# Performance work log

Measured on AMD Instinct MI355X. Metric: run time of the kernel, lower is better.

Reference implementation:

```python
import jax, jax.numpy as jnp
import numpy as np

H = 16   # num_heads
G = 4    # groups (code structurally requires 4)
DIM = 1024
HD = DIM // H // G  # 16


def setup_inputs() -> dict:
    key = jax.random.key(0)
    k1, k2, k3 = jax.random.split(key, 3)
    x = jax.random.normal(k1, (8, 4096, DIM), dtype=jnp.float32)
    w_qkvw = jax.random.normal(k2, (DIM, 4 * DIM), dtype=jnp.float32) * 0.02
    w_out = jax.random.normal(k3, (DIM, DIM), dtype=jnp.float32) * 0.02
    return {"x": x, "w_qkvw": w_qkvw, "w_out": w_out}


def reference(x, w_qkvw, w_out):
    B, S, dim = x.shape
    qkvw = x @ w_qkvw  # [B, S, 4*dim]
    # chunk into G groups along last dim -> G tensors of [B, S, dim] (G==4)
    chunks = jnp.split(qkvw, G, axis=-1)
    # each chunk split again into G sub-chunks of [B, S, dim/G]
    subs = [jnp.split(t, G, axis=-1) for t in chunks]
    # torch: q,k,v,w = [cat([qi,ki,vi,wi], dim=0) for qi,ki,vi,wi in zip(*subs)]
    q = jnp.concatenate([subs[i][0] for i in range(4)], axis=0)  # [4B, S, dim/G]
    k = jnp.concatenate([subs[i][1] for i in range(4)], axis=0)
    v = jnp.concatenate([subs[i][2] for i in range(4)], axis=0)
    w = jnp.concatenate([subs[i][3] for i in range(4)], axis=0)
    # faithful row-major reshape: [4B, S, dim/G] -> [4B, H, S, hd] -> transpose(1,2)
    def shp(t):
        return t.reshape(B * G, H, -1, HD).swapaxes(1, 2)  # [4B, S, H, hd]
    q, k, v = shp(q), shp(k), shp(v)
    w = w.reshape(B * G, H, -1, HD)  # [4B, H, S, hd]
    scale = HD ** -0.5
    scores = (q @ k.swapaxes(-2, -1)) * scale          # [4B, S, H, H]
    attn = jax.nn.softmax(scores, axis=-1)
    o = (attn @ v).swapaxes(1, 2).reshape(B, S, dim)   # [B, S, dim]
    return (o * w.reshape(B, S, dim)) @ w_out
```

## Files before the change

kernel.cpp:

```cpp
#include <hip/hip_runtime.h>
#include <hip/hip_bf16.h>
#include <stdint.h>


typedef __bf16 bf16;
typedef __bf16 bf16x8 __attribute__((ext_vector_type(8)));
typedef float f32x4 __attribute__((ext_vector_type(4)));

__device__ __forceinline__ void gload16(const bf16* g, bf16* l) {
  __builtin_amdgcn_global_load_lds(
      (const __attribute__((address_space(1))) void*)g,
      (__attribute__((address_space(3))) void*)l, 16, 0, 0);
}

#define BAR() __builtin_amdgcn_s_barrier()
#define SB() __builtin_amdgcn_sched_barrier(0)
#define LGKM0 asm volatile("s_waitcnt lgkmcnt(0)" ::: "memory")
#define VM6 asm volatile("s_waitcnt vmcnt(6)" ::: "memory")
#define VM0 asm volatile("s_waitcnt vmcnt(0)" ::: "memory")
#define PRIO1 __builtin_amdgcn_s_setprio(1)
#define PRIO0 __builtin_amdgcn_s_setprio(0)

#define READ_A8(dst, base, mq)                                                \
  {                                                                           \
    _Pragma("unroll") for (int i = 0; i < 4; ++i)                             \
        _Pragma("unroll") for (int kk = 0; kk < 2; ++kk)                      \
            dst[i][kk] = *(const bf16x8*)(lds + (base) + ahalf +              \
                                          ((mq)*64 + i * 16 + fr) * 128 +     \
                                          ((kk * 64 + fkb) ^ xo));            \
  }
#define READ_B4(dst, base, nh)                                                \
  {                                                                           \
    _Pragma("unroll") for (int j2 = 0; j2 < 2; ++j2)                          \
        _Pragma("unroll") for (int kk = 0; kk < 2; ++kk)                      \
            dst[j2][kk] = *(const bf16x8*)(lds + (base) + bhalf +             \
                                           (bro + (nh)*32 + j2 * 16 + fr) * 128 + \
                                           ((kk * 64 + fkb) ^ xo));           \
  }
#define MFMA_Q(arr, bv, mq, nh)                                               \
  {                                                                           \
    _Pragma("unroll") for (int i = 0; i < 4; ++i)                             \
        _Pragma("unroll") for (int j2 = 0; j2 < 2; ++j2) {                    \
      acc[(mq)*4 + i][(nh)*2 + j2] = __builtin_amdgcn_mfma_f32_16x16x32_bf16( \
          arr[i][0], bv[j2][0], acc[(mq)*4 + i][(nh)*2 + j2], 0, 0, 0);       \
      acc[(mq)*4 + i][(nh)*2 + j2] = __builtin_amdgcn_mfma_f32_16x16x32_bf16( \
          arr[i][1], bv[j2][1], acc[(mq)*4 + i][(nh)*2 + j2], 0, 0, 0);       \
    }                                                                         \
  }
#define STAGE(gsrc, lbase)                                                    \
  {                                                                           \
    gload16((gsrc), (bf16*)(lds + (lbase) + wv * 1024));                      \
    gload16((gsrc) + 64 * 1024, (bf16*)(lds + (lbase) + 8192 + wv * 1024));   \
  }

template <typename OutT>
__global__ __launch_bounds__(512, 2)
void gemm256(const bf16* __restrict__ A, const bf16* __restrict__ BT,
             OutT* __restrict__ C, int N, int super) {
  constexpr int K = 1024;
  __shared__ __align__(16) char smem[131072];
  char* lds = smem;

  const int tid = threadIdx.x;
  const int lane = tid & 63;
  const int wv = tid >> 6;
  const int wr = wv >> 2;
  const int wc = wv & 3;

  const int gx = gridDim.x;
  const int nwg = gx * gridDim.y;
  const int bid = blockIdx.y * gx + blockIdx.x;
  const int xcd = bid & 7;
  const int l = bid >> 3;
  long trow, tcol;
  if (super) {
    const int s = l >> 5, i = l & 31;
    const int colS = gx >> 2;
    trow = xcd * 16 + (s / colS) * 8 + (i >> 2);
    tcol = (s % colS) * 4 + (i & 3);
  } else {
    const int swz = xcd * (nwg >> 3) + l;
    trow = swz / gx;
    tcol = swz % gx;
  }
  const long row0 = trow * 256;
  const long col0 = tcol * 256;

  const int srow = tid >> 3;
  const int scol = (((tid & 7) * 16) ^ ((srow & 7) << 4)) >> 1;
  const bf16* gA = A + (row0 + srow) * K + scol;
  const bf16* gB = BT + (col0 + srow) * K + scol;

  const int fr = lane & 15;
  const int fkb = (lane >> 4) * 16;
  const int xo = (fr & 7) << 4;
  const int bro = (wc & 1) * 64;
  const int ahalf = wr * 16384;
  const int bhalf = (wc >> 1) * 16384;

  bf16x8 a0[4][2], a1[4][2], bn0[2][2], bn1[2][2];
  f32x4 acc[8][4] = {};

  STAGE(gA, 0); STAGE(gA + 131072, 16384);
  STAGE(gB, 65536); STAGE(gB + 131072, 81920);
  STAGE(gB + 64, 98304); STAGE(gB + 131072 + 64, 114688);
  STAGE(gA + 64, 32768);
  VM6;
  BAR();

  const bf16* gAm = gA;
  const bf16* gBm = gB;
  for (int j = 0; j < 8; ++j) {
    const bool nl = (j < 7);
    READ_B4(bn0, 65536, 0);
    STAGE(gAm + 131072 + 64, 49152);
    BAR(); LGKM0; SB();
    if (j) { PRIO1; MFMA_Q(a1, bn1, 1, 1); PRIO0; }
    BAR();
    READ_A8(a0, 0, 0);
    READ_B4(bn1, 65536, 1);
    BAR(); LGKM0; SB();
    PRIO1; MFMA_Q(a0, bn0, 0, 0); PRIO0;
    BAR();
    READ_A8(a1, 0, 1);
    if (nl) { STAGE(gBm + 128, 65536); STAGE(gBm + 131072 + 128, 81920); }
    BAR(); LGKM0; SB();
    PRIO1; MFMA_Q(a1, bn0, 1, 0); PRIO0;
    BAR();
    if (nl) {
      STAGE(gAm + 128, 0);
      VM6;
    } else {
      VM0;
    }
    BAR(); LGKM0; SB();
    PRIO1; MFMA_Q(a0, bn1, 0, 1); PRIO0;
    BAR();
    READ_B4(bn0, 98304, 0);
    if (nl) STAGE(gAm + 131072 + 128, 16384);
    BAR(); LGKM0; SB();
    PRIO1; MFMA_Q(a1, bn1, 1, 1); PRIO0;
    BAR();
    READ_A8(a0, 32768, 0);
    READ_B4(bn1, 98304, 1);
    BAR(); LGKM0; SB();
    PRIO1; MFMA_Q(a0, bn0, 0, 0); PRIO0;
    BAR();
    READ_A8(a1, 32768, 1);
    if (nl) STAGE(gBm + 192, 98304);
    BAR(); LGKM0; SB();
    PRIO1; MFMA_Q(a1, bn0, 1, 0); PRIO0;
    BAR();
    if (nl) {
      STAGE(gBm + 131072 + 192, 114688);
      STAGE(gAm + 192, 32768);
      VM6;
    }
    BAR(); LGKM0; SB();
    PRIO1; MFMA_Q(a0, bn1, 0, 1); PRIO0;
    BAR();
    gAm += 128;
    gBm += 128;
  }
  PRIO1; MFMA_Q(a1, bn1, 1, 1); PRIO0;

  const int crow = (lane >> 4) * 4;
  const int ccol = lane & 15;
  const long rb = row0 + wr * 128;
  const long cb = col0 + wc * 64;
#pragma unroll
  for (int m = 0; m < 8; ++m)
#pragma unroll
    for (int n = 0; n < 4; ++n)
#pragma unroll
      for (int i = 0; i < 4; ++i)
        C[(rb + m * 16 + crow + i) * (long)N + cb + n * 16 + ccol] =
            (OutT)acc[m][n][i];
}

__device__ __forceinline__ void load16f(const bf16* p, float* f) {
  const uint4* u = (const uint4*)p;
  uint4 a = u[0], b = u[1];
  uint32_t w[8] = {a.x, a.y, a.z, a.w, b.x, b.y, b.z, b.w};
#pragma unroll
  for (int j = 0; j < 8; ++j) {
    f[2 * j] = __uint_as_float(w[j] << 16);
    f[2 * j + 1] = __uint_as_float(w[j] & 0xffff0000u);
  }
}

__global__ __launch_bounds__(256)
void attn_fuse(const bf16* __restrict__ qkvw, bf16* __restrict__ ow,
               int b0, long bstride) {
  __shared__ bf16 data[16 * 1024];
  const int s_hi = blockIdx.x;
  const int g = blockIdx.y;
  const int bz = blockIdx.z;
  const int b = b0 + bz;
  const bf16* base = qkvw + (long)bz * bstride;
  const int tid = threadIdx.x;

#pragma unroll
  for (int i = 0; i < 8; ++i) {
    int c = tid + i * 256;
    int h = c >> 7;
    int col = (c & 127) * 8;
    *(uint4*)&data[h * 1024 + col] =
        *(const uint4*)(base + (long)(h * 256 + s_hi) * 4096 + g * 1024 + col);
  }
  __syncthreads();

  const int s_lo = tid >> 4;
  const int h1 = tid & 15;
  const int off = s_lo * 16;

  float q[16], p[16], o[16];
  load16f(&data[h1 * 1024 + off], q);

  float mx = -1e30f;
#pragma unroll
  for (int h2 = 0; h2 < 16; ++h2) {
    float kf[16];
    load16f(&data[h2 * 1024 + 256 + off], kf);
    float s = 0.f;
#pragma unroll
    for (int d = 0; d < 16; ++d) s += q[d] * kf[d];
    s *= 0.25f;
    p[h2] = s;
    mx = fmaxf(mx, s);
  }
  float sum = 0.f;
#pragma unroll
  for (int h2 = 0; h2 < 16; ++h2) {
    float e = __expf(p[h2] - mx);
    p[h2] = e;
    sum += e;
  }
  const float inv = 1.f / sum;
#pragma unroll
  for (int d = 0; d < 16; ++d) o[d] = 0.f;
#pragma unroll
  for (int h2 = 0; h2 < 16; ++h2) {
    float vf[16];
    load16f(&data[h2 * 1024 + 512 + off], vf);
    const float av = p[h2] * inv;
#pragma unroll
    for (int d = 0; d < 16; ++d) o[d] += av * vf[d];
  }
  float wf[16];
  load16f(&data[h1 * 1024 + 768 + off], wf);

  const int bp = g * 8 + b;
  const long R = (long)(bp >> 2) * 4096 + (bp & 3) * 1024 + h1 * 64 + (s_hi >> 2);
  const int cbo = (s_hi & 3) * 256 + off;
  union { uint4 u[2]; bf16 hh[16]; } st;
#pragma unroll
  for (int d = 0; d < 16; ++d) st.hh[d] = (bf16)(o[d] * wf[d]);
  uint4* dst = (uint4*)&ow[R * 1024 + cbo];
  dst[0] = st.u[0];
  dst[1] = st.u[1];
}

__global__ __launch_bounds__(256)
void cast_x_kernel(const float* __restrict__ in, bf16* __restrict__ out, long n4) {
  long i = (long)blockIdx.x * 256 + threadIdx.x;
  if (i >= n4) return;
  float4 v = ((const float4*)in)[i];
  union { uint2 d; bf16 h[4]; } r;
  r.h[0] = (bf16)v.x; r.h[1] = (bf16)v.y; r.h[2] = (bf16)v.z; r.h[3] = (bf16)v.w;
  ((uint2*)out)[i] = r.d;
}

__global__ __launch_bounds__(256)
void tcast_kernel(const float* __restrict__ in, bf16* __restrict__ out, int R, int C) {
  __shared__ float t[64][65];
  const int c0 = blockIdx.x * 64, r0 = blockIdx.y * 64;
  const int lr = threadIdx.x >> 6;
  const int lc = threadIdx.x & 63;
#pragma unroll
  for (int i = 0; i < 16; ++i)
    t[lr + i * 4][lc] = in[(long)(r0 + lr + i * 4) * C + c0 + lc];
  __syncthreads();
#pragma unroll
  for (int i = 0; i < 16; ++i) {
    int oc = lr + i * 4;
    out[(long)(c0 + oc) * R + r0 + lc] = (bf16)t[lc][oc];
  }
}

extern "C" void kernel_launch(void* const* d_in, const int* in_sizes, int n_in,
                              void* d_out, int out_size, void* d_ws, size_t ws_size,
                              hipStream_t stream) {
  const float* x = (const float*)d_in[0];
  const float* w_qkvw = (const float*)d_in[1];
  const float* w_out = (const float*)d_in[2];
  float* out = (float*)d_out;

  char* ws = (char*)d_ws;
  size_t off = 0;
  bf16* x_bf = (bf16*)(ws + off); off += (size_t)32768 * 1024 * 2;
  bf16* bt1  = (bf16*)(ws + off); off += (size_t)4096 * 1024 * 2;
  bf16* bt2  = (bf16*)(ws + off); off += (size_t)1024 * 1024 * 2;
  bf16* owb  = (bf16*)(ws + off); off += (size_t)32768 * 1024 * 2;
  bf16* qk   = (bf16*)(ws + off);
  const size_t rem = ws_size > off ? ws_size - off : 0;
  const size_t full_need = (size_t)32768 * 4096 * 2;

  cast_x_kernel<<<32768, 256, 0, stream>>>(x, x_bf, (long)8388608);
  tcast_kernel<<<dim3(64, 16), 256, 0, stream>>>(w_qkvw, bt1, 1024, 4096);
  tcast_kernel<<<dim3(16, 16), 256, 0, stream>>>(w_out, bt2, 1024, 1024);

  if (rem >= full_need) {
    gemm256<bf16><<<dim3(16, 128), 512, 0, stream>>>(x_bf, bt1, qk, 4096, 1);
    attn_fuse<<<dim3(256, 4, 8), 256, 0, stream>>>(qk, owb, 0, (long)4096 * 4096);
  } else {
    for (int b = 0; b < 8; ++b) {
      gemm256<bf16><<<dim3(16, 16), 512, 0, stream>>>(
          x_bf + (size_t)b * 4096 * 1024, bt1, qk, 4096, 0);
      attn_fuse<<<dim3(256, 4, 1), 256, 0, stream>>>(qk, owb, b, 0);
    }
  }
  gemm256<float><<<dim3(4, 128), 512, 0, stream>>>(owb, bt2, out, 1024, 1);
}
```

Measured before the change: 506.2 us.

## Restructure GEMM main loop with fewer barriers and partial LDS waitcnts

Reorders the K-loop so all A fragments for a half-tile are read up front, uses partial lgkmcnt waits (8/4/0) so MFMAs start before every LDS read completes, and removes about half the workgroup barriers. The global-to-LDS staging order is reshuffled, with B's second half now prefetched inside the loop and vmcnt lowered to 4. This cuts synchronization stalls and improves overlap of LDS reads with MFMA, but the tighter buffer reuse risks LDS read/write hazards and higher register pressure.

```diff
diff --git a/kernel.cpp b/kernel.cpp
--- a/kernel.cpp
+++ b/kernel.cpp
@@ -15,8 +15,10 @@
 
 #define BAR() __builtin_amdgcn_s_barrier()
 #define SB() __builtin_amdgcn_sched_barrier(0)
+#define LGKM8 asm volatile("s_waitcnt lgkmcnt(8)" ::: "memory")
+#define LGKM4 asm volatile("s_waitcnt lgkmcnt(4)" ::: "memory")
 #define LGKM0 asm volatile("s_waitcnt lgkmcnt(0)" ::: "memory")
-#define VM6 asm volatile("s_waitcnt vmcnt(6)" ::: "memory")
+#define VM4 asm volatile("s_waitcnt vmcnt(4)" ::: "memory")
 #define VM0 asm volatile("s_waitcnt vmcnt(0)" ::: "memory")
 #define PRIO1 __builtin_amdgcn_s_setprio(1)
 #define PRIO0 __builtin_amdgcn_s_setprio(0)
@@ -103,66 +105,64 @@
 
   STAGE(gA, 0); STAGE(gA + 131072, 16384);
   STAGE(gB, 65536); STAGE(gB + 131072, 81920);
-  STAGE(gB + 64, 98304); STAGE(gB + 131072 + 64, 114688);
-  STAGE(gA + 64, 32768);
-  VM6;
-  BAR();
+  STAGE(gA + 64, 32768); STAGE(gA + 131072 + 64, 49152);
+  VM4;
 
   const bf16* gAm = gA;
   const bf16* gBm = gB;
   for (int j = 0; j < 8; ++j) {
     const bool nl = (j < 7);
+    BAR();
     READ_B4(bn0, 65536, 0);
-    STAGE(gAm + 131072 + 64, 49152);
-    BAR(); LGKM0; SB();
-    if (j) { PRIO1; MFMA_Q(a1, bn1, 1, 1); PRIO0; }
-    BAR();
     READ_A8(a0, 0, 0);
+    READ_A8(a1, 0, 1);
+    STAGE(gBm + 64, 98304);
+    LGKM8; SB();
+    PRIO1; MFMA_Q(a0, bn0, 0, 0); PRIO0;
+    BAR();
     READ_B4(bn1, 65536, 1);
-    BAR(); LGKM0; SB();
-    PRIO1; MFMA_Q(a0, bn0, 0, 0); PRIO0;
-    BAR();
-    READ_A8(a1, 0, 1);
-    if (nl) { STAGE(gBm + 128, 65536); STAGE(gBm + 131072 + 128, 81920); }
-    BAR(); LGKM0; SB();
+    STAGE(gBm + 131072 + 64, 114688);
+    LGKM4; SB();
     PRIO1; MFMA_Q(a1, bn0, 1, 0); PRIO0;
     BAR();
+    if (nl) STAGE(gAm + 128, 0);
+    LGKM0; SB();
+    PRIO1; MFMA_Q(a1, bn1, 1, 1); PRIO0;
+    BAR();
     if (nl) {
-      STAGE(gAm + 128, 0);
-      VM6;
+      STAGE(gAm + 131072 + 128, 16384);
+      VM4;
     } else {
       VM0;
     }
-    BAR(); LGKM0; SB();
+    SB();
     PRIO1; MFMA_Q(a0, bn1, 0, 1); PRIO0;
     BAR();
     READ_B4(bn0, 98304, 0);
-    if (nl) STAGE(gAm + 131072 + 128, 16384);
-    BAR(); LGKM0; SB();
+    READ_A8(a0, 32768, 0);
+    READ_A8(a1, 32768, 1);
+    if (nl) STAGE(gBm + 128, 65536);
+    LGKM8; SB();
+    PRIO1; MFMA_Q(a0, bn0, 0, 0); PRIO0;
+    BAR();
+    READ_B4(bn1, 98304, 1);
+    if (nl) STAGE(gBm + 131072 + 128, 81920);
+    LGKM4; SB();
+    PRIO1; MFMA_Q(a1, bn0, 1, 0); PRIO0;
+    BAR();
+    if (nl) STAGE(gAm + 192, 32768);
+    LGKM0; SB();
     PRIO1; MFMA_Q(a1, bn1, 1, 1); PRIO0;
     BAR();
-    READ_A8(a0, 32768, 0);
-    READ_B4(bn1, 98304, 1);
-    BAR(); LGKM0; SB();
-    PRIO1; MFMA_Q(a0, bn0, 0, 0); PRIO0;
-    BAR();
-    READ_A8(a1, 32768, 1);
-    if (nl) STAGE(gBm + 192, 98304);
-    BAR(); LGKM0; SB();
-    PRIO1; MFMA_Q(a1, bn0, 1, 0); PRIO0;
-    BAR();
     if (nl) {
-      STAGE(gBm + 131072 + 192, 114688);
-      STAGE(gAm + 192, 32768);
-      VM6;
+      STAGE(gAm + 131072 + 192, 49152);
+      VM4;
     }
-    BAR(); LGKM0; SB();
+    SB();
     PRIO1; MFMA_Q(a0, bn1, 0, 1); PRIO0;
-    BAR();
     gAm += 128;
     gBm += 128;
   }
-  PRIO1; MFMA_Q(a1, bn1, 1, 1); PRIO0;
 
   const int crow = (lane >> 4) * 4;
   const int ccol = lane & 15;
```

After: 452.9 us (median of 2 runs). 10.5% less time.
